# Kernel tuning notes

Measured on AMD Instinct MI355X. Metric: run time of the kernel, lower is better.

## Reference

```python
import jax, jax.numpy as jnp
import numpy as np

B, S, D, H = 2, 2048, 1024, 16

def setup_inputs() -> dict:
    key = jax.random.key(0)
    k_x, k_wq, k_bq, k_wk, k_wv = jax.random.split(key, 5)
    return {
        "x": jax.random.normal(k_x, (B, S, D), dtype=jnp.float32),
        "Wq": jax.random.normal(k_wq, (D, D), dtype=jnp.float32) / 100.0,
        "Bq": jax.random.normal(k_bq, (1, D), dtype=jnp.float32) / 100.0,
        "Wk": jax.random.normal(k_wk, (D, D), dtype=jnp.float32) / 100.0,
        "Wv": jax.random.normal(k_wv, (D, D), dtype=jnp.float32) / 100.0,
        "n_heads": H,
    }

def reference(x, Wq, Bq, Wk, Wv, n_heads):
    b, s, d = x.shape
    dh = d // n_heads
    # Projections
    Q = x @ Wq + Bq          # [b, s, d]
    K = x @ Wk               # [b, s, d]
    V = x @ Wv               # [b, s, d]
    # Unconventional head split: last dim -> (d_head, n_heads), heads LAST
    Q = Q.reshape(b, s, dh, n_heads)
    K = K.reshape(b, s, dh, n_heads)
    V = V.reshape(b, s, dh, n_heads)
    # NOTE: original scales by sqrt(d_model), not sqrt(d_head)
    scale = 1.0 / np.sqrt(d).astype(np.float32)
    scores = jnp.einsum('bidh,bjdh->bijh', Q, K) * scale  # [b, i, j, h]
    attn = jax.nn.softmax(scores, axis=2)                 # softmax over j
    out = jnp.einsum('bijh,bjdh->bidh', attn, V)          # [b, i, dh, h]
    return out.reshape(b, s, d)                            # merge_heads
```

## Files before the change

kernel.cpp:

```cpp
#include <hip/hip_runtime.h>

#define B_ 2
#define S_ 2048
#define D_ 1024
#define H_ 16

typedef __attribute__((ext_vector_type(8))) short short8;
typedef __attribute__((ext_vector_type(8))) unsigned short ushort8;
typedef __attribute__((ext_vector_type(4))) short short4v;
typedef __attribute__((ext_vector_type(4))) float f32x4;

__device__ __forceinline__ unsigned short f2b(float f){
  unsigned u = __float_as_uint(f);
  u += 0x7fffu + ((u >> 16) & 1u);
  return (unsigned short)(u >> 16);
}
__device__ __forceinline__ float b2f(unsigned short b){
  return __uint_as_float(((unsigned)b) << 16);
}
__device__ __forceinline__ float fast_exp2(float x){
#if __has_builtin(__builtin_amdgcn_exp2f)
  return __builtin_amdgcn_exp2f(x);
#else
  return exp2f(x);
#endif
}
__device__ __forceinline__ unsigned pack_trunc(unsigned u_lo, unsigned u_hi){
#if __has_builtin(__builtin_amdgcn_perm)
  return __builtin_amdgcn_perm(u_hi, u_lo, 0x07060302u);
#else
  return (u_lo >> 16) | (u_hi & 0xffff0000u);
#endif
}
__device__ __forceinline__ f32x4 mfma16(short8 a, short8 b, f32x4 c){
  return __builtin_amdgcn_mfma_f32_16x16x32_bf16(a, b, c, 0, 0, 0);
}
__device__ __forceinline__ f32x4 mfma16k16(short4v a, short4v b, f32x4 c){
#if __has_builtin(__builtin_amdgcn_mfma_f32_16x16x16bf16_1k)
  return __builtin_amdgcn_mfma_f32_16x16x16bf16_1k(a, b, c, 0, 0, 0);
#else
  asm("v_mfma_f32_16x16x16_bf16 %0, %1, %2, %0" : "+v"(c) : "v"(a), "v"(b));
  return c;
#endif
}
__device__ __forceinline__ void gload_lds16(const void* g, void* l){
  __builtin_amdgcn_global_load_lds((const __attribute__((address_space(1))) unsigned int*)g,
                                   (__attribute__((address_space(3))) unsigned int*)l, 16, 0, 0);
}

__global__ __launch_bounds__(256) void convert_x(const float* __restrict__ x,
                                                 unsigned short* __restrict__ xbf){
  int i = (blockIdx.x * 256 + threadIdx.x) * 8;
  f32x4 a = *(const f32x4*)(x + i);
  f32x4 b = *(const f32x4*)(x + i + 4);
  ushort8 o;
  o[0]=f2b(a[0]); o[1]=f2b(a[1]); o[2]=f2b(a[2]); o[3]=f2b(a[3]);
  o[4]=f2b(b[0]); o[5]=f2b(b[1]); o[6]=f2b(b[2]); o[7]=f2b(b[3]);
  *(ushort8*)(xbf + i) = o;
}

__global__ __launch_bounds__(256) void transpose_w(const float* __restrict__ Wq,
                                                   const float* __restrict__ Wk,
                                                   const float* __restrict__ Wv,
                                                   unsigned short* __restrict__ wT){
  int z = blockIdx.z;
  const float* W = (z == 0) ? Wq : ((z == 1) ? Wk : Wv);
  __shared__ float tile[32][33];
  int nb = blockIdx.x * 32, kb = blockIdx.y * 32;
  int tx = threadIdx.x & 31, ty = threadIdx.x >> 5;
  #pragma unroll
  for (int it = 0; it < 4; it++){
    int row = ty + it * 8;
    tile[row][tx] = W[(size_t)(kb + row) * D_ + nb + tx];
  }
  __syncthreads();
  unsigned short* outp = wT + (size_t)z * D_ * D_;
  #pragma unroll
  for (int it = 0; it < 4; it++){
    int row = ty + it * 8;
    int n = nb + row;
    int np = ((n & 15) << 6) | (n >> 4);
    outp[(size_t)np * D_ + kb + tx] = f2b(tile[tx][row]);
  }
}

__global__ __launch_bounds__(256) void qkv_gemm(const unsigned short* __restrict__ xbf,
                                                const unsigned short* __restrict__ wT,
                                                const float* __restrict__ Bq,
                                                unsigned short* __restrict__ qatt,
                                                unsigned short* __restrict__ katt,
                                                unsigned short* __restrict__ vatt){
  __shared__ char SM[34816];
  unsigned short* Ct = (unsigned short*)SM;
  const int proj = blockIdx.z;
  const int mbase = blockIdx.y * 128, nbase = blockIdx.x * 128;
  const unsigned short* bsrc = wT + (size_t)proj * D_ * D_;
  const int t = threadIdx.x, w = t >> 6, lane = t & 63, ln = lane & 15, hi = lane >> 4;
  const int wr = w >> 1, wc = w & 1;
  const int srow = t >> 2, scol = (t & 3) << 3;
  f32x4 acc[4][4] = {};

  #pragma unroll
  for (int i = 0; i < 2; i++){
    gload_lds16(xbf  + (size_t)(mbase + srow + i * 64) * D_ + scol, SM + w * 1024 + i * 4096);
    gload_lds16(bsrc + (size_t)(nbase + srow + i * 64) * D_ + scol, SM + 8192 + w * 1024 + i * 4096);
  }
  __syncthreads();

  int cur = 0;
  for (int ks = 0; ks < D_; ks += 32){
    if (ks + 32 < D_){
      char* nb_ = SM + (cur ^ 1) * 16384;
      #pragma unroll
      for (int i = 0; i < 2; i++){
        gload_lds16(xbf  + (size_t)(mbase + srow + i * 64) * D_ + ks + 32 + scol, nb_ + w * 1024 + i * 4096);
        gload_lds16(bsrc + (size_t)(nbase + srow + i * 64) * D_ + ks + 32 + scol, nb_ + 8192 + w * 1024 + i * 4096);
      }
    }
    const unsigned short* At = (const unsigned short*)(SM + cur * 16384);
    const unsigned short* Bt = (const unsigned short*)(SM + cur * 16384 + 8192);
    short8 af[4], bf[4];
    #pragma unroll
    for (int q = 0; q < 4; q++) af[q] = *(const short8*)&At[(wr * 64 + q * 16 + ln) * 32 + hi * 8];
    #pragma unroll
    for (int p = 0; p < 4; p++) bf[p] = *(const short8*)&Bt[(wc * 64 + p * 16 + ln) * 32 + hi * 8];
    #pragma unroll
    for (int q = 0; q < 4; q++)
      #pragma unroll
      for (int p = 0; p < 4; p++)
        acc[q][p] = mfma16(af[q], bf[p], acc[q][p]);
    __syncthreads();
    cur ^= 1;
  }

  const float qscale = 0.04508422002778011f;
  const int b = mbase >> 11, ms = mbase & 2047;

  if (proj == 2){
    #pragma unroll
    for (int p = 0; p < 4; p++)
      #pragma unroll
      for (int q = 0; q < 4; q++)
        #pragma unroll
        for (int r = 0; r < 4; r++)
          Ct[(wc*64 + p*16 + ln) * 136 + wr*64 + q*16 + hi*4 + r] = f2b(acc[q][p][r]);
    __syncthreads();
    #pragma unroll
    for (int j = 0; j < 8; j++){
      int u = j * 256 + t;
      int col = u >> 4, s0 = (u & 15) * 8;
      int h = blockIdx.x * 2 + (col >> 6), r = col & 63;
      short8 v = *(const short8*)&Ct[col * 136 + s0];
      *(short8*)&vatt[((size_t)(b*16 + h) * 64 + r) * 2048 + ms + s0] = v;
    }
  } else {
    const int hglob = blockIdx.x * 2 + wc;
    #pragma unroll
    for (int p = 0; p < 4; p++){
      float bqv = (proj == 0) ? Bq[(p*16 + ln)*16 + hglob] : 0.f;
      #pragma unroll
      for (int q = 0; q < 4; q++)
        #pragma unroll
        for (int r = 0; r < 4; r++){
          float v = acc[q][p][r];
          if (proj == 0) v = (v + bqv) * qscale;
          Ct[(wr*64 + q*16 + hi*4 + r) * 136 + wc*64 + p*16 + ln] = f2b(v);
        }
    }
    __syncthreads();
    unsigned short* dstb = (proj == 0) ? qatt : katt;
    #pragma unroll
    for (int j = 0; j < 8; j++){
      int u = j * 256 + t;
      int hl = u >> 10, rem = u & 1023, sl = rem >> 3, r0 = (rem & 7) * 8;
      int h = blockIdx.x * 2 + hl;
      short8 v = *(const short8*)&Ct[sl * 136 + hl*64 + r0];
      *(short8*)&dstb[((size_t)(b*16 + h) * 2048 + ms + sl) * 64 + r0] = v;
    }
  }
}

template<int NS>
__global__ __launch_bounds__(256) void attn_fwd(const unsigned short* __restrict__ qatt,
                                                const unsigned short* __restrict__ katt,
                                                const unsigned short* __restrict__ vatt,
                                                unsigned short* __restrict__ pnum,
                                                float* __restrict__ pden){
  __shared__ unsigned short Kt[2][64 * 64];
  __shared__ unsigned short Vt[2][64 * 64];
  const int t = threadIdx.x, w = t >> 6, lane = t & 63, ln = lane & 15, hi = lane >> 4;
  const int bid = blockIdx.x;
  const int bpx = (512 * NS) / 8;
  const int L = (bid & 7) * bpx + (bid >> 3);
  const int bh = L / (16 * NS);
  const int rem = L % (16 * NS);
  const int z = rem >> 4, qc = rem & 15;
  const int b = bh >> 4, h = bh & 15;
  const int q0 = qc * 128 + w * 32;
  const int kvbase = z * (S_ / NS);
  const int NT = (S_ / NS) / 64;
  const unsigned short* Qh = qatt + (size_t)bh * S_ * 64;
  const unsigned short* Kh = katt + (size_t)bh * S_ * 64;
  const unsigned short* Vh = vatt + (size_t)bh * 64 * S_;

  short8 qf[2][2];
  #pragma unroll
  for (int qb = 0; qb < 2; qb++)
    #pragma unroll
    for (int kc = 0; kc < 2; kc++)
      qf[qb][kc] = *(const short8*)&Qh[(size_t)(q0 + qb * 16 + ln) * 64 + kc * 32 + hi * 8];

  const int srow = w * 16 + (lane >> 3);
  const int scol0 = ((lane & 7) * 16) ^ ((srow & 7) << 4);
  const int scol1 = ((lane & 7) * 16) ^ (((srow + 8) & 7) << 4);

  f32x4 acc[2][4] = {};
  f32x4 accd[2] = {};
  const short4v vones = {(short)0x3F80, (short)0x3F80, (short)0x3F80, (short)0x3F80};

  {
    int kv = kvbase;
    gload_lds16(Kh + (size_t)(kv + srow) * 64 + (scol0 >> 1),     (char*)&Kt[0][0] + w * 2048);
    gload_lds16(Kh + (size_t)(kv + srow + 8) * 64 + (scol1 >> 1), (char*)&Kt[0][0] + w * 2048 + 1024);
    gload_lds16(Vh + (size_t)srow * S_ + kv + (scol0 >> 1),       (char*)&Vt[0][0] + w * 2048);
    gload_lds16(Vh + (size_t)(srow + 8) * S_ + kv + (scol1 >> 1), (char*)&Vt[0][0] + w * 2048 + 1024);
  }
  __syncthreads();

  int cur = 0;
  for (int tt = 0; tt < NT; ++tt){
    if (tt + 1 < NT){
      int kv = kvbase + (tt + 1) * 64;
      int nb = cur ^ 1;
      gload_lds16(Kh + (size_t)(kv + srow) * 64 + (scol0 >> 1),     (char*)&Kt[nb][0] + w * 2048);
      gload_lds16(Kh + (size_t)(kv + srow + 8) * 64 + (scol1 >> 1), (char*)&Kt[nb][0] + w * 2048 + 1024);
      gload_lds16(Vh + (size_t)srow * S_ + kv + (scol0 >> 1),       (char*)&Vt[nb][0] + w * 2048);
      gload_lds16(Vh + (size_t)(srow + 8) * S_ + kv + (scol1 >> 1), (char*)&Vt[nb][0] + w * 2048 + 1024);
    }
    const unsigned short* Kc = &Kt[cur][0];
    const unsigned short* Vc = &Vt[cur][0];

    short8 kf[4][2];
    #pragma unroll
    for (int kb = 0; kb < 4; kb++)
      #pragma unroll
      for (int kc = 0; kc < 2; kc++){
        int eb = (((kc * 64 + hi * 16) ^ ((ln & 7) << 4)) >> 1);
        kf[kb][kc] = *(const short8*)&Kc[(kb * 16 + ln) * 64 + eb];
      }

    short4v pa[2][4];
    #pragma unroll
    for (int qb = 0; qb < 2; qb++)
      #pragma unroll
      for (int kb = 0; kb < 4; kb++){
        f32x4 zz = {0.f, 0.f, 0.f, 0.f};
        zz = mfma16(kf[kb][0], qf[qb][0], zz);
        zz = mfma16(kf[kb][1], qf[qb][1], zz);
        unsigned u0 = __float_as_uint(fast_exp2(zz[0]));
        unsigned u1 = __float_as_uint(fast_exp2(zz[1]));
        unsigned u2 = __float_as_uint(fast_exp2(zz[2]));
        unsigned u3 = __float_as_uint(fast_exp2(zz[3]));
        union { unsigned u[2]; short4v s; } pk;
        pk.u[0] = pack_trunc(u0, u1);
        pk.u[1] = pack_trunc(u2, u3);
        pa[qb][kb] = pk.s;
      }

    #pragma unroll
    for (int kb = 0; kb < 4; kb++){
      accd[0] = mfma16k16(pa[0][kb], vones, accd[0]);
      accd[1] = mfma16k16(pa[1][kb], vones, accd[1]);
    }

    #pragma unroll
    for (int cb = 0; cb < 4; cb++)
      #pragma unroll
      for (int kb = 0; kb < 4; kb++){
        int eb = (((kb * 32 + hi * 8) ^ ((ln & 7) << 4)) >> 1);
        short4v vf = *(const short4v*)&Vc[(cb * 16 + ln) * 64 + eb];
        acc[0][cb] = mfma16k16(pa[0][kb], vf, acc[0][cb]);
        acc[1][cb] = mfma16k16(pa[1][kb], vf, acc[1][cb]);
      }
    __syncthreads();
    cur ^= 1;
  }

  if (ln == 0){
    #pragma unroll
    for (int qb = 0; qb < 2; qb++)
      #pragma unroll
      for (int r = 0; r < 4; r++)
        pden[((size_t)(z * 2 + b) * S_ + q0 + qb * 16 + hi * 4 + r) * 16 + h] = accd[qb][r];
  }

  const size_t rowb = (size_t)(z * 2 + b) * S_;
  #pragma unroll
  for (int qb = 0; qb < 2; qb++)
    #pragma unroll
    for (int cb = 0; cb < 4; cb++)
      #pragma unroll
      for (int r = 0; r < 4; r++){
        int qrow = q0 + qb * 16 + hi * 4 + r;
        pnum[(rowb + qrow) * 1024 + h * 64 + cb * 16 + ln] = f2b(acc[qb][cb][r]);
      }
}

template<int NSPLIT>
__global__ __launch_bounds__(256) void attn_reduce(const unsigned short* __restrict__ pnum,
                                                   const float* __restrict__ pden,
                                                   float* __restrict__ out){
  __shared__ float L[4 * 1056];
  const int t = threadIdx.x;
  const int row_l = t >> 6, lane = t & 63;
  const int grow = blockIdx.x * 4 + row_l;
  const int e0 = lane * 16;
  const int h = e0 >> 6;
  float den = 0.f;
  float nsum[16];
  #pragma unroll
  for (int j = 0; j < 16; j++) nsum[j] = 0.f;
  #pragma unroll
  for (int z = 0; z < NSPLIT; z++){
    const size_t prow = (size_t)z * 4096 + grow;
    den += pden[prow * 16 + h];
    #pragma unroll
    for (int c = 0; c < 2; c++){
      ushort8 nv = *(const ushort8*)&pnum[prow * 1024 + e0 + c * 8];
      #pragma unroll
      for (int k = 0; k < 8; k++) nsum[c*8 + k] += b2f(nv[k]);
    }
  }
  float rinv = 1.0f / den;
  #pragma unroll
  for (int j = 0; j < 16; j++){
    int col = e0 + j;
    L[row_l * 1056 + col + (col >> 5)] = nsum[j] * rinv;
  }
  __syncthreads();
  const int d0 = lane * 16;
  #pragma unroll
  for (int c = 0; c < 4; c++){
    f32x4 o;
    #pragma unroll
    for (int k = 0; k < 4; k++){
      int d = d0 + c * 4 + k;
      int e = ((d & 15) << 6) | (d >> 4);
      o[k] = L[row_l * 1056 + e + (e >> 5)];
    }
    *(f32x4*)&out[(size_t)grow * 1024 + d0 + c * 4] = o;
  }
}

extern "C" void kernel_launch(void* const* d_in, const int* in_sizes, int n_in,
                              void* d_out, int out_size, void* d_ws, size_t ws_size,
                              hipStream_t stream){
  const float* x  = (const float*)d_in[0];
  const float* Wq = (const float*)d_in[1];
  const float* Bq = (const float*)d_in[2];
  const float* Wk = (const float*)d_in[3];
  const float* Wv = (const float*)d_in[4];
  char* ws = (char*)d_ws;
  const size_t MB = 1024 * 1024;
  unsigned short* qatt = (unsigned short*)(ws);
  unsigned short* katt = (unsigned short*)(ws + 8 * MB);
  unsigned short* vatt = (unsigned short*)(ws + 16 * MB);
  unsigned short* xbf  = (unsigned short*)(ws + 24 * MB);
  unsigned short* wT   = (unsigned short*)(ws + 32 * MB);
  float* outp = (float*)d_out;

  convert_x<<<2048, 256, 0, stream>>>(x, xbf);
  transpose_w<<<dim3(32, 32, 3), 256, 0, stream>>>(Wq, Wk, Wv, wT);
  qkv_gemm<<<dim3(8, 32, 3), 256, 0, stream>>>(xbf, wT, Bq, qatt, katt, vatt);

  if (ws_size >= 59 * MB){
    const int NS = 4;
    unsigned short* pnum = (unsigned short*)(ws + 24 * MB);
    float* pden = (float*)(ws + 24 * MB + (size_t)NS * 8 * MB);
    attn_fwd<NS><<<512 * NS, 256, 0, stream>>>(qatt, katt, vatt, pnum, pden);
    attn_reduce<NS><<<1024, 256, 0, stream>>>(pnum, pden, outp);
  } else if (ws_size >= 42 * MB){
    const int NS = 2;
    unsigned short* pnum = (unsigned short*)(ws + 24 * MB);
    float* pden = (float*)(ws + 24 * MB + (size_t)NS * 8 * MB);
    attn_fwd<NS><<<512 * NS, 256, 0, stream>>>(qatt, katt, vatt, pnum, pden);
    attn_reduce<NS><<<1024, 256, 0, stream>>>(pnum, pden, outp);
  } else {
    const int NS = 1;
    unsigned short* pnum = (unsigned short*)(ws + 24 * MB);
    float* pden = (float*)(ws + 24 * MB + (size_t)NS * 8 * MB);
    attn_fwd<NS><<<512 * NS, 256, 0, stream>>>(qatt, katt, vatt, pnum, pden);
    attn_reduce<NS><<<1024, 256, 0, stream>>>(pnum, pden, outp);
  }
}
```

Baseline: 104.7 us.

## Double query rows per wave in attention and interleave K-tile compute

Each attention block now covers 256 query rows (64 per wave) instead of 128, halving the grid so every K/V tile loaded into LDS is reused across twice as many queries. The per-tile loop is restructured to iterate over key blocks outermost, loading K fragments per kb and immediately doing the score, exp, denominator and PV MFMAs, so the full pa[][] array no longer has to stay live. This cuts global and LDS traffic per FLOP, at the cost of larger accumulators (64 floats of acc per lane), more register pressure and fewer blocks in flight.

```diff
diff --git a/kernel.cpp b/kernel.cpp
--- a/kernel.cpp
+++ b/kernel.cpp
@@ -190,22 +190,22 @@
   __shared__ unsigned short Vt[2][64 * 64];
   const int t = threadIdx.x, w = t >> 6, lane = t & 63, ln = lane & 15, hi = lane >> 4;
   const int bid = blockIdx.x;
-  const int bpx = (512 * NS) / 8;
+  const int bpx = (256 * NS) / 8;
   const int L = (bid & 7) * bpx + (bid >> 3);
-  const int bh = L / (16 * NS);
-  const int rem = L % (16 * NS);
-  const int z = rem >> 4, qc = rem & 15;
+  const int bh = L / (8 * NS);
+  const int rem = L % (8 * NS);
+  const int z = rem >> 3, qc = rem & 7;
   const int b = bh >> 4, h = bh & 15;
-  const int q0 = qc * 128 + w * 32;
+  const int q0 = qc * 256 + w * 64;
   const int kvbase = z * (S_ / NS);
   const int NT = (S_ / NS) / 64;
   const unsigned short* Qh = qatt + (size_t)bh * S_ * 64;
   const unsigned short* Kh = katt + (size_t)bh * S_ * 64;
   const unsigned short* Vh = vatt + (size_t)bh * 64 * S_;
 
-  short8 qf[2][2];
-  #pragma unroll
-  for (int qb = 0; qb < 2; qb++)
+  short8 qf[4][2];
+  #pragma unroll
+  for (int qb = 0; qb < 4; qb++)
     #pragma unroll
     for (int kc = 0; kc < 2; kc++)
       qf[qb][kc] = *(const short8*)&Qh[(size_t)(q0 + qb * 16 + ln) * 64 + kc * 32 + hi * 8];
@@ -214,8 +214,8 @@
   const int scol0 = ((lane & 7) * 16) ^ ((srow & 7) << 4);
   const int scol1 = ((lane & 7) * 16) ^ (((srow + 8) & 7) << 4);
 
-  f32x4 acc[2][4] = {};
-  f32x4 accd[2] = {};
+  f32x4 acc[4][4] = {};
+  f32x4 accd[4] = {};
   const short4v vones = {(short)0x3F80, (short)0x3F80, (short)0x3F80, (short)0x3F80};
 
   {
@@ -240,23 +240,19 @@
     const unsigned short* Kc = &Kt[cur][0];
     const unsigned short* Vc = &Vt[cur][0];
 
-    short8 kf[4][2];
-    #pragma unroll
-    for (int kb = 0; kb < 4; kb++)
-      #pragma unroll
-      for (int kc = 0; kc < 2; kc++){
-        int eb = (((kc * 64 + hi * 16) ^ ((ln & 7) << 4)) >> 1);
-        kf[kb][kc] = *(const short8*)&Kc[(kb * 16 + ln) * 64 + eb];
-      }
-
-    short4v pa[2][4];
-    #pragma unroll
-    for (int qb = 0; qb < 2; qb++)
-      #pragma unroll
-      for (int kb = 0; kb < 4; kb++){
+    #pragma unroll
+    for (int kb = 0; kb < 4; kb++){
+      const int eb0 = (((0 * 64 + hi * 16) ^ ((ln & 7) << 4)) >> 1);
+      const int eb1 = (((1 * 64 + hi * 16) ^ ((ln & 7) << 4)) >> 1);
+      short8 kf0 = *(const short8*)&Kc[(kb * 16 + ln) * 64 + eb0];
+      short8 kf1 = *(const short8*)&Kc[(kb * 16 + ln) * 64 + eb1];
+
+      short4v pa[4];
+      #pragma unroll
+      for (int qb = 0; qb < 4; qb++){
         f32x4 zz = {0.f, 0.f, 0.f, 0.f};
-        zz = mfma16(kf[kb][0], qf[qb][0], zz);
-        zz = mfma16(kf[kb][1], qf[qb][1], zz);
+        zz = mfma16(kf0, qf[qb][0], zz);
+        zz = mfma16(kf1, qf[qb][1], zz);
         unsigned u0 = __float_as_uint(fast_exp2(zz[0]));
         unsigned u1 = __float_as_uint(fast_exp2(zz[1]));
         unsigned u2 = __float_as_uint(fast_exp2(zz[2]));
@@ -264,31 +260,26 @@
         union { unsigned u[2]; short4v s; } pk;
         pk.u[0] = pack_trunc(u0, u1);
         pk.u[1] = pack_trunc(u2, u3);
-        pa[qb][kb] = pk.s;
+        pa[qb] = pk.s;
+        accd[qb] = mfma16k16(pa[qb], vones, accd[qb]);
       }
 
-    #pragma unroll
-    for (int kb = 0; kb < 4; kb++){
-      accd[0] = mfma16k16(pa[0][kb], vones, accd[0]);
-      accd[1] = mfma16k16(pa[1][kb], vones, accd[1]);
-    }
-
-    #pragma unroll
-    for (int cb = 0; cb < 4; cb++)
-      #pragma unroll
-      for (int kb = 0; kb < 4; kb++){
+      #pragma unroll
+      for (int cb = 0; cb < 4; cb++){
         int eb = (((kb * 32 + hi * 8) ^ ((ln & 7) << 4)) >> 1);
         short4v vf = *(const short4v*)&Vc[(cb * 16 + ln) * 64 + eb];
-        acc[0][cb] = mfma16k16(pa[0][kb], vf, acc[0][cb]);
-        acc[1][cb] = mfma16k16(pa[1][kb], vf, acc[1][cb]);
+        #pragma unroll
+        for (int qb = 0; qb < 4; qb++)
+          acc[qb][cb] = mfma16k16(pa[qb], vf, acc[qb][cb]);
       }
+    }
     __syncthreads();
     cur ^= 1;
   }
 
   if (ln == 0){
     #pragma unroll
-    for (int qb = 0; qb < 2; qb++)
+    for (int qb = 0; qb < 4; qb++)
       #pragma unroll
       for (int r = 0; r < 4; r++)
         pden[((size_t)(z * 2 + b) * S_ + q0 + qb * 16 + hi * 4 + r) * 16 + h] = accd[qb][r];
@@ -296,7 +287,7 @@
 
   const size_t rowb = (size_t)(z * 2 + b) * S_;
   #pragma unroll
-  for (int qb = 0; qb < 2; qb++)
+  for (int qb = 0; qb < 4; qb++)
     #pragma unroll
     for (int cb = 0; cb < 4; cb++)
       #pragma unroll
@@ -377,19 +368,19 @@
     const int NS = 4;
     unsigned short* pnum = (unsigned short*)(ws + 24 * MB);
     float* pden = (float*)(ws + 24 * MB + (size_t)NS * 8 * MB);
-    attn_fwd<NS><<<512 * NS, 256, 0, stream>>>(qatt, katt, vatt, pnum, pden);
+    attn_fwd<NS><<<256 * NS, 256, 0, stream>>>(qatt, katt, vatt, pnum, pden);
     attn_reduce<NS><<<1024, 256, 0, stream>>>(pnum, pden, outp);
   } else if (ws_size >= 42 * MB){
     const int NS = 2;
     unsigned short* pnum = (unsigned short*)(ws + 24 * MB);
     float* pden = (float*)(ws + 24 * MB + (size_t)NS * 8 * MB);
-    attn_fwd<NS><<<512 * NS, 256, 0, stream>>>(qatt, katt, vatt, pnum, pden);
+    attn_fwd<NS><<<256 * NS, 256, 0, stream>>>(qatt, katt, vatt, pnum, pden);
     attn_reduce<NS><<<1024, 256, 0, stream>>>(pnum, pden, outp);
   } else {
     const int NS = 1;
     unsigned short* pnum = (unsigned short*)(ws + 24 * MB);
     float* pden = (float*)(ws + 24 * MB + (size_t)NS * 8 * MB);
-    attn_fwd<NS><<<512 * NS, 256, 0, stream>>>(qatt, katt, vatt, pnum, pden);
+    attn_fwd<NS><<<256 * NS, 256, 0, stream>>>(qatt, katt, vatt, pnum, pden);
     attn_reduce<NS><<<1024, 256, 0, stream>>>(pnum, pden, outp);
   }
 }
```

Result: slower. 113.8 us (+8.7%).
